# Performance work log

Hardware: AMD Instinct MI355X
Metric: run time of the kernel (lower is better)

The kernel has to match this reference:

```python
import jax, jax.numpy as jnp
import numpy as np

N_NODES = 100000
N_EDGES = 2000000


def _mlp3(h, w1, b1, w2, b2, w3, b3):
    h = jax.nn.relu(h @ w1.T + b1)
    h = jax.nn.relu(h @ w2.T + b2)
    return h @ w3.T + b3


def setup_inputs() -> dict:
    key = jax.random.key(0)
    ks = jax.random.split(key, 24)
    inp = {
        "x": jax.random.normal(ks[0], (N_NODES, 3), dtype=jnp.float32),
        "edge_index": jax.random.randint(ks[1], (2, N_EDGES), 0, N_NODES, dtype=jnp.int64),
        "edge_attr": jax.random.normal(ks[2], (N_EDGES, 4), dtype=jnp.float32),
    }
    # MLP params (PyTorch Linear: y = x @ W.T + b)
    shapes = {
        "r1_w1": (40, 10), "r1_b1": (40,), "r1_w2": (40, 40), "r1_b2": (40,), "r1_w3": (4, 40), "r1_b3": (4,),
        "o_w1": (40, 7), "o_b1": (40,), "o_w2": (40, 40), "o_b2": (40,), "o_w3": (3, 40), "o_b3": (3,),
        "r2_w1": (40, 10), "r2_b1": (40,), "r2_w2": (40, 40), "r2_b2": (40,), "r2_w3": (1, 40), "r2_b3": (1,),
    }
    for i, (name, shp) in enumerate(shapes.items()):
        inp[name] = jax.random.normal(ks[3 + i], shp, dtype=jnp.float32) * 0.1
    return inp


def reference(x, edge_index, edge_attr,
              r1_w1, r1_b1, r1_w2, r1_b2, r1_w3, r1_b3,
              o_w1, o_b1, o_w2, o_b2, o_w3, o_b3,
              r2_w1, r2_b1, r2_w2, r2_b2, r2_w3, r2_b3):
    n = x.shape[0]
    src, dst = edge_index[0], edge_index[1]  # x_j <- src, x_i <- dst
    # message: relational MLP R1 over [x_i, x_j, edge_attr]  -> [E,4]
    m1 = jnp.concatenate([x[dst], x[src], edge_attr], axis=1)
    e_msg = _mlp3(m1, r1_w1, r1_b1, r1_w2, r1_b2, r1_w3, r1_b3)
    # aggregate: scatter-add messages to destination nodes -> [N,4]
    aggr = jax.ops.segment_sum(e_msg, dst, num_segments=n)
    # update: object MLP O over [x, aggr] -> [N,3]
    x_tilde = _mlp3(jnp.concatenate([x, aggr], axis=1), o_w1, o_b1, o_w2, o_b2, o_w3, o_b3)
    # edge classifier R2 over [x_tilde_i, x_tilde_j, E] -> sigmoid [E,1]
    m2 = jnp.concatenate([x_tilde[dst], x_tilde[src], e_msg], axis=1)
    return jax.nn.sigmoid(_mlp3(m2, r2_w1, r2_b1, r2_w2, r2_b2, r2_w3, r2_b3))
```

## Files before the change

kernel.cpp:

```cpp
#include <hip/hip_runtime.h>
#include <math.h>


typedef __fp16 hf8 __attribute__((ext_vector_type(8)));
typedef _Float16 f16x2 __attribute__((ext_vector_type(2)));
typedef float f32x16 __attribute__((ext_vector_type(16)));
typedef unsigned u32x4 __attribute__((ext_vector_type(4)));

#define NEPC  64
#define BS    4096

__device__ __forceinline__ f32x16 mfma16(hf8 a, hf8 b, f32x16 c) {
    return __builtin_amdgcn_mfma_f32_32x32x16_f16(a, b, c, 0, 0, 0);
}
__device__ __forceinline__ unsigned pk2(float a, float b) {
    return __builtin_bit_cast(unsigned, __builtin_amdgcn_cvt_pkrtz(a, b));
}
__device__ __forceinline__ unsigned pk2_relu(float a, float b) {
    return __builtin_bit_cast(unsigned,
        __builtin_amdgcn_cvt_pkrtz(fmaxf(a, 0.f), fmaxf(b, 0.f)));
}
__device__ __forceinline__ unsigned pswap(unsigned v) {
    return (unsigned)__shfl_xor((int)v, 32, 64);
}
__device__ __forceinline__ hf8 frag_from(unsigned a, unsigned b, unsigned c, unsigned d) {
    u32x4 v = {a, b, c, d};
    return __builtin_bit_cast(hf8, v);
}

__device__ __forceinline__ void build_frags(const f32x16& t0, const f32x16& t1,
                                            int hi, hf8& F0, hf8& F1, hf8& F2) {
    const unsigned w0 = pk2_relu(t0[0],  t0[1]);
    const unsigned w1 = pk2_relu(t0[2],  t0[3]);
    const unsigned w2 = pk2_relu(t0[4],  t0[5]);
    const unsigned w3 = pk2_relu(t0[6],  t0[7]);
    const unsigned w4 = pk2_relu(t0[8],  t0[9]);
    const unsigned w5 = pk2_relu(t0[10], t0[11]);
    const unsigned w6 = pk2_relu(t0[12], t0[13]);
    const unsigned w7 = pk2_relu(t0[14], t0[15]);
    const unsigned w8 = pk2_relu(t1[0],  t1[1]);
    const unsigned w9 = pk2_relu(t1[2],  t1[3]);
    const unsigned p0 = pswap(w0), p1 = pswap(w1), p2 = pswap(w2), p3 = pswap(w3);
    const unsigned p4 = pswap(w4), p5 = pswap(w5), p6 = pswap(w6), p7 = pswap(w7);
    const unsigned p8 = pswap(w8), p9 = pswap(w9);
    F0 = frag_from(hi ? p2 : w0, hi ? p3 : w1, hi ? w2 : p0, hi ? w3 : p1);
    F1 = frag_from(hi ? p6 : w4, hi ? p7 : w5, hi ? w6 : p4, hi ? w7 : p5);
    F2 = frag_from(hi ? 0x00003c00u : w8, hi ? 0u : w9, hi ? 0u : p8, hi ? 0u : p9);
}

template<int IN, int OUT>
__device__ hf8 load_wfrag(const float* __restrict__ w, const float* __restrict__ b,
                          int mt, int ks, int lane) {
    const int r = mt * 32 + (lane & 31);
    const int kbase = ks * 16 + ((lane >> 5) & 1) * 8;
    hf8 f;
#pragma unroll
    for (int j = 0; j < 8; ++j) {
        const int k = kbase + j;
        float v = 0.f;
        if (r < OUT) {
            if (k < IN) v = w[r * IN + k];
            else if (k == IN) v = b[r];
        }
        f[j] = (__fp16)v;
    }
    return f;
}

template<int OUT>
__device__ hf8 load_wfrag_l1(const float* __restrict__ w, const float* __restrict__ b,
                             int mt, int lane) {
    const int r = mt * 32 + (lane & 31);
    const int kbase = ((lane >> 5) & 1) * 8;
    hf8 f;
#pragma unroll
    for (int j = 0; j < 8; ++j) {
        const int k = kbase + j;
        float v = 0.f;
        if (r < OUT) {
            int src = -1;
            if (k < 3) src = k;
            else if (k >= 4 && k < 7) src = k - 1;
            else if (k >= 8 && k < 12) src = k - 2;
            if (src >= 0) v = w[r * 10 + src];
            else if (k == 12) v = b[r];
        }
        f[j] = (__fp16)v;
    }
    return f;
}

template<bool IS_MSG>
__global__ __launch_bounds__(256, 2) void edge_kernel(
    const uint2* __restrict__ nodef,
    const int*   __restrict__ ei,
    const void*  __restrict__ eattr,
    const float* __restrict__ w1, const float* __restrict__ b1,
    const float* __restrict__ w2, const float* __restrict__ b2,
    const float* __restrict__ w3, const float* __restrict__ b3,
    uint2* __restrict__ emsg_out,
    float* __restrict__ out,
    int n_edges)
{
    const int lane = threadIdx.x & 63;
    const int ecol = lane & 31;
    const int hi = lane >> 5;

    hf8 wa1[2], wa2[2][3], wa3[3];
#pragma unroll
    for (int t = 0; t < 2; ++t) wa1[t] = load_wfrag_l1<40>(w1, b1, t, lane);
#pragma unroll
    for (int t = 0; t < 2; ++t)
#pragma unroll
        for (int s = 0; s < 3; ++s) wa2[t][s] = load_wfrag<40, 40>(w2, b2, t, s, lane);
#pragma unroll
    for (int s = 0; s < 3; ++s)
        wa3[s] = load_wfrag<40, (IS_MSG ? 4 : 1)>(w3, b3, 0, s, lane);

    const int gwave = (int)((blockIdx.x * blockDim.x + threadIdx.x) >> 6);
    const int nwave = (int)((gridDim.x * blockDim.x) >> 6);
    const int nchunk = (n_edges + NEPC - 1) / NEPC;
    const int last = n_edges - 1;

    int c = gwave;
    if (c >= nchunk) return;
    auto eclampX = [&](int cc) { int e = cc * NEPC + ecol;      return e < last ? e : last; };
    auto eclampY = [&](int cc) { int e = cc * NEPC + 32 + ecol; return e < last ? e : last; };

    uint2 fAX, fBX, fAY, fBY;
    int sNX = 0, dNX = 0, sNY = 0, dNY = 0;
    {
        const int eX = eclampX(c), eY = eclampY(c);
        if (hi == 0) {
            const int sX = ei[eX], dX = ei[n_edges + eX];
            const int sY = ei[eY], dY = ei[n_edges + eY];
            fAX = nodef[dX]; fBX = nodef[sX];
            fAY = nodef[dY]; fBY = nodef[sY];
            const int e2X = eclampX(c + nwave), e2Y = eclampY(c + nwave);
            sNX = ei[e2X]; dNX = ei[n_edges + e2X];
            sNY = ei[e2Y]; dNY = ei[n_edges + e2Y];
        } else {
            if (IS_MSG) {
                const float4 evX = ((const float4*)eattr)[eX];
                fAX = make_uint2(pk2(evX.x, evX.y), pk2(evX.z, evX.w));
                const float4 evY = ((const float4*)eattr)[eY];
                fAY = make_uint2(pk2(evY.x, evY.y), pk2(evY.z, evY.w));
            } else {
                fAX = ((const uint2*)eattr)[eX];
                fAY = ((const uint2*)eattr)[eY];
            }
            fBX = make_uint2(0x00003c00u, 0u);
            fBY = fBX;
        }
    }

    for (; c < nchunk; ) {
        const int cn = c + nwave;

        const hf8 bfX = frag_from(fAX.x, fAX.y, fBX.x, fBX.y);
        const hf8 bfY = frag_from(fAY.x, fAY.y, fBY.x, fBY.y);

        uint2 nfAX = fAX, nfBX = fBX, nfAY = fAY, nfBY = fBY;
        int sPX = sNX, dPX = dNX, sPY = sNY, dPY = dNY;
        {
            if (hi == 0) {
                nfAX = nodef[dNX]; nfBX = nodef[sNX];
                nfAY = nodef[dNY]; nfBY = nodef[sNY];
                const int e3X = eclampX(cn + nwave), e3Y = eclampY(cn + nwave);
                sPX = ei[e3X]; dPX = ei[n_edges + e3X];
                sPY = ei[e3Y]; dPY = ei[n_edges + e3Y];
            } else {
                const int e2X = eclampX(cn), e2Y = eclampY(cn);
                if (IS_MSG) {
                    const float4 evX = ((const float4*)eattr)[e2X];
                    nfAX = make_uint2(pk2(evX.x, evX.y), pk2(evX.z, evX.w));
                    const float4 evY = ((const float4*)eattr)[e2Y];
                    nfAY = make_uint2(pk2(evY.x, evY.y), pk2(evY.z, evY.w));
                } else {
                    nfAX = ((const uint2*)eattr)[e2X];
                    nfAY = ((const uint2*)eattr)[e2Y];
                }
            }
        }

        f32x16 a0X = {}, a1X = {}, a0Y = {}, a1Y = {};
        a0X = mfma16(wa1[0], bfX, a0X);
        a0Y = mfma16(wa1[0], bfY, a0Y);
        a1X = mfma16(wa1[1], bfX, a1X);
        a1Y = mfma16(wa1[1], bfY, a1Y);

        hf8 f0X, f1X, f2X, f0Y, f1Y, f2Y;
        build_frags(a0X, a1X, hi, f0X, f1X, f2X);
        build_frags(a0Y, a1Y, hi, f0Y, f1Y, f2Y);

        f32x16 c0X = {}, c1X = {}, c0Y = {}, c1Y = {};
        c0X = mfma16(wa2[0][0], f0X, c0X); c0Y = mfma16(wa2[0][0], f0Y, c0Y);
        c1X = mfma16(wa2[1][0], f0X, c1X); c1Y = mfma16(wa2[1][0], f0Y, c1Y);
        c0X = mfma16(wa2[0][1], f1X, c0X); c0Y = mfma16(wa2[0][1], f1Y, c0Y);
        c1X = mfma16(wa2[1][1], f1X, c1X); c1Y = mfma16(wa2[1][1], f1Y, c1Y);
        c0X = mfma16(wa2[0][2], f2X, c0X); c0Y = mfma16(wa2[0][2], f2Y, c0Y);
        c1X = mfma16(wa2[1][2], f2X, c1X); c1Y = mfma16(wa2[1][2], f2Y, c1Y);

        hf8 g0X, g1X, g2X, g0Y, g1Y, g2Y;
        build_frags(c0X, c1X, hi, g0X, g1X, g2X);
        build_frags(c0Y, c1Y, hi, g0Y, g1Y, g2Y);

        f32x16 z0X = {}, z0Y = {};
        z0X = mfma16(wa3[0], g0X, z0X); z0Y = mfma16(wa3[0], g0Y, z0Y);
        z0X = mfma16(wa3[1], g1X, z0X); z0Y = mfma16(wa3[1], g1Y, z0Y);
        z0X = mfma16(wa3[2], g2X, z0X); z0Y = mfma16(wa3[2], g2Y, z0Y);

        if (hi == 0) {
            const int eX = c * NEPC + ecol;
            const int eY = eX + 32;
            if (eX < n_edges) {
                if (IS_MSG)
                    emsg_out[eX] = make_uint2(pk2(z0X[0], z0X[1]), pk2(z0X[2], z0X[3]));
                else
                    out[eX] = 1.f / (1.f + expf(-z0X[0]));
            }
            if (eY < n_edges) {
                if (IS_MSG)
                    emsg_out[eY] = make_uint2(pk2(z0Y[0], z0Y[1]), pk2(z0Y[2], z0Y[3]));
                else
                    out[eY] = 1.f / (1.f + expf(-z0Y[0]));
            }
        }

        fAX = nfAX; fBX = nfBX; fAY = nfAY; fBY = nfBY;
        sNX = sPX; dNX = dPX; sNY = sPY; dNY = dPY;
        c = cn;
    }
}

__global__ __launch_bounds__(256) void nodef_kernel(
    const float* __restrict__ x, uint2* __restrict__ nodef, int n_nodes)
{
    int n = blockIdx.x * blockDim.x + threadIdx.x;
    if (n >= n_nodes) return;
    nodef[n] = make_uint2(pk2(x[n * 3 + 0], x[n * 3 + 1]), pk2(x[n * 3 + 2], 0.f));
}

__device__ __forceinline__ void bin_accum(float* __restrict__ bin, int bbase, int d,
                                          const uint2* __restrict__ emsg, long long e) {
    const unsigned nl = (unsigned)(d - bbase);
    if (nl < (unsigned)BS) {
        const uint2 mv = emsg[e];
        f16x2 lo = __builtin_bit_cast(f16x2, mv.x);
        f16x2 hi = __builtin_bit_cast(f16x2, mv.y);
        float* p = bin + nl * 4;
        atomicAdd(p + 0, (float)lo.x);
        atomicAdd(p + 1, (float)lo.y);
        atomicAdd(p + 2, (float)hi.x);
        atomicAdd(p + 3, (float)hi.y);
    }
}

__global__ __launch_bounds__(1024) void bin_kernel(
    const int* __restrict__ ei,
    const uint2* __restrict__ emsg,
    float* __restrict__ scratch,
    int n_edges, int nw)
{
    __shared__ float bin[BS * 4];
    const int B = gridDim.x / nw;
    const int wchunk = blockIdx.x / B;
    const int b = blockIdx.x % B;
    const int bbase = b * BS;
    const int tid = threadIdx.x;

#pragma unroll
    for (int i = 0; i < (BS * 4) / 1024; ++i)
        bin[tid + i * 1024] = 0.f;
    __syncthreads();

    long long e0 = ((long long)n_edges * wchunk / nw) & ~3LL;
    long long e1 = (wchunk == nw - 1) ? (long long)n_edges
                                      : (((long long)n_edges * (wchunk + 1) / nw) & ~3LL);
    const long long nfull = (e1 - e0) >> 2;
    const int* dstp = ei + n_edges;

    for (long long g = tid; g < nfull; g += 1024) {
        const long long e = e0 + g * 4;
        const int4 d4 = *(const int4*)(dstp + e);
        bin_accum(bin, bbase, d4.x, emsg, e + 0);
        bin_accum(bin, bbase, d4.y, emsg, e + 1);
        bin_accum(bin, bbase, d4.z, emsg, e + 2);
        bin_accum(bin, bbase, d4.w, emsg, e + 3);
    }
    for (long long e = e0 + nfull * 4 + tid; e < e1; e += 1024)
        bin_accum(bin, bbase, dstp[e], emsg, e);

    __syncthreads();

    float4* dst = (float4*)(scratch + ((size_t)(b * nw + wchunk)) * BS * 4);
    const float4* srcb = (const float4*)bin;
#pragma unroll
    for (int i = 0; i < (BS * 4) / 4 / 1024; ++i)
        dst[tid + i * 1024] = srcb[tid + i * 1024];
}

__global__ __launch_bounds__(256) void reduce_kernel(
    const float* __restrict__ scratch,
    float* __restrict__ aggr,
    int n_nodes, int nw)
{
    int n = blockIdx.x * blockDim.x + threadIdx.x;
    if (n >= n_nodes) return;
    const int b = n / BS, nl = n % BS;
    float4 acc = make_float4(0.f, 0.f, 0.f, 0.f);
    for (int w = 0; w < nw; ++w) {
        const float4 v = *(const float4*)(scratch + ((size_t)(b * nw + w) * BS + nl) * 4);
        acc.x += v.x; acc.y += v.y; acc.z += v.z; acc.w += v.w;
    }
    *(float4*)(aggr + (size_t)n * 4) = acc;
}

template<int IN, int OUT, bool RELU>
__device__ __forceinline__ void dense(const float* __restrict__ w,
                                      const float* __restrict__ b,
                                      const float* in, float* out) {
#pragma unroll
    for (int j = 0; j < OUT; ++j) {
        float acc = b[j];
#pragma unroll
        for (int k = 0; k < IN; ++k) acc = fmaf(w[j * IN + k], in[k], acc);
        out[j] = RELU ? fmaxf(acc, 0.f) : acc;
    }
}

__global__ __launch_bounds__(256) void node_kernel(
    const float* __restrict__ x,
    const float* __restrict__ aggr,
    const float* __restrict__ w1, const float* __restrict__ b1,
    const float* __restrict__ w2, const float* __restrict__ b2,
    const float* __restrict__ w3, const float* __restrict__ b3,
    uint2* __restrict__ xth,
    int n_nodes)
{
    int n = blockIdx.x * blockDim.x + threadIdx.x;
    if (n >= n_nodes) return;

    float in[7];
    in[0] = x[n * 3 + 0]; in[1] = x[n * 3 + 1]; in[2] = x[n * 3 + 2];
    const float4 ag = *(const float4*)(aggr + (size_t)n * 4);
    in[3] = ag.x; in[4] = ag.y; in[5] = ag.z; in[6] = ag.w;

    float h1[40], h2[40], o[3];
    dense<7, 40, true >(w1, b1, in, h1);
    dense<40, 40, true>(w2, b2, h1, h2);
    dense<40, 3, false>(w3, b3, h2, o);

    xth[n] = make_uint2(pk2(o[0], o[1]), pk2(o[2], 0.f));
}

extern "C" void kernel_launch(void* const* d_in, const int* in_sizes, int n_in,
                              void* d_out, int out_size, void* d_ws, size_t ws_size,
                              hipStream_t stream) {
    const float* x  = (const float*)d_in[0];
    const int*   ei = (const int*)d_in[1];
    const float* ea = (const float*)d_in[2];

    const float* r1_w1 = (const float*)d_in[3];
    const float* r1_b1 = (const float*)d_in[4];
    const float* r1_w2 = (const float*)d_in[5];
    const float* r1_b2 = (const float*)d_in[6];
    const float* r1_w3 = (const float*)d_in[7];
    const float* r1_b3 = (const float*)d_in[8];

    const float* o_w1 = (const float*)d_in[9];
    const float* o_b1 = (const float*)d_in[10];
    const float* o_w2 = (const float*)d_in[11];
    const float* o_b2 = (const float*)d_in[12];
    const float* o_w3 = (const float*)d_in[13];
    const float* o_b3 = (const float*)d_in[14];

    const float* r2_w1 = (const float*)d_in[15];
    const float* r2_b1 = (const float*)d_in[16];
    const float* r2_w2 = (const float*)d_in[17];
    const float* r2_b2 = (const float*)d_in[18];
    const float* r2_w3 = (const float*)d_in[19];
    const float* r2_b3 = (const float*)d_in[20];

    const int n_nodes = in_sizes[0] / 3;
    const int n_edges = in_sizes[2] / 4;
    const int B = (n_nodes + BS - 1) / BS;

    uint2* nodef   = (uint2*)d_ws;
    float* aggr    = (float*)(nodef + n_nodes);
    uint2* emsg    = (uint2*)(aggr + (size_t)n_nodes * 4);
    float* scratch = (float*)(emsg + n_edges);

    const size_t fixed_bytes = (size_t)n_nodes * 8 + (size_t)n_nodes * 16
                             + (size_t)n_edges * 8;
    int nw = 16;
    if (ws_size < fixed_bytes + (size_t)B * nw * BS * 4 * sizeof(float)) nw = 8;

    const int eb = 512;
    const int nb = (n_nodes + 255) / 256;

    nodef_kernel<<<nb, 256, 0, stream>>>(x, nodef, n_nodes);

    edge_kernel<true><<<eb, 256, 0, stream>>>(nodef, ei, (const void*)ea,
        r1_w1, r1_b1, r1_w2, r1_b2, r1_w3, r1_b3,
        emsg, nullptr, n_edges);

    bin_kernel<<<B * nw, 1024, 0, stream>>>(ei, emsg, scratch, n_edges, nw);

    reduce_kernel<<<nb, 256, 0, stream>>>(scratch, aggr, n_nodes, nw);

    node_kernel<<<nb, 256, 0, stream>>>(x, aggr,
        o_w1, o_b1, o_w2, o_b2, o_w3, o_b3, nodef, n_nodes);

    edge_kernel<false><<<eb, 256, 0, stream>>>(nodef, ei, (const void*)emsg,
        r2_w1, r2_b1, r2_w2, r2_b2, r2_w3, r2_b3,
        nullptr, (float*)d_out, n_edges);
}
```

Before: 195.3 us.

## Replace filtered scan binning with counting-sort bucketing before shared-memory scatter-add

```diff
diff --git a/kernel.cpp b/kernel.cpp
--- a/kernel.cpp
+++ b/kernel.cpp
@@ -9,6 +9,7 @@
 
 #define NEPC  64
 #define BS    4096
+#define NBMAX 32
 
 __device__ __forceinline__ f32x16 mfma16(hf8 a, hf8 b, f32x16 c) {
     return __builtin_amdgcn_mfma_f32_32x32x16_f16(a, b, c, 0, 0, 0);
@@ -233,6 +234,11 @@
     }
 }
 
+__global__ __launch_bounds__(64) void zero_small(unsigned* __restrict__ p, int n) {
+    int i = threadIdx.x;
+    if (i < n) p[i] = 0u;
+}
+
 __global__ __launch_bounds__(256) void nodef_kernel(
     const float* __restrict__ x, uint2* __restrict__ nodef, int n_nodes)
 {
@@ -241,59 +247,112 @@
     nodef[n] = make_uint2(pk2(x[n * 3 + 0], x[n * 3 + 1]), pk2(x[n * 3 + 2], 0.f));
 }
 
-__device__ __forceinline__ void bin_accum(float* __restrict__ bin, int bbase, int d,
-                                          const uint2* __restrict__ emsg, long long e) {
-    const unsigned nl = (unsigned)(d - bbase);
-    if (nl < (unsigned)BS) {
-        const uint2 mv = emsg[e];
-        f16x2 lo = __builtin_bit_cast(f16x2, mv.x);
-        f16x2 hi = __builtin_bit_cast(f16x2, mv.y);
-        float* p = bin + nl * 4;
+__global__ __launch_bounds__(1024) void count_kernel(
+    const int* __restrict__ dstp, unsigned* __restrict__ counts, int n_edges)
+{
+    __shared__ unsigned lc[NBMAX];
+    if (threadIdx.x < NBMAX) lc[threadIdx.x] = 0u;
+    __syncthreads();
+    const int stride = gridDim.x * 1024;
+    for (int e = blockIdx.x * 1024 + threadIdx.x; e < n_edges; e += stride)
+        atomicAdd(&lc[((unsigned)dstp[e]) >> 12], 1u);
+    __syncthreads();
+    if (threadIdx.x < NBMAX && lc[threadIdx.x])
+        atomicAdd(&counts[threadIdx.x], lc[threadIdx.x]);
+}
+
+__global__ __launch_bounds__(1024) void split_kernel(
+    const int* __restrict__ dstp,
+    const uint2* __restrict__ emsg,
+    const unsigned* __restrict__ counts,
+    unsigned* __restrict__ cursor,
+    unsigned* __restrict__ buckets,
+    int n_edges, int nbins)
+{
+    __shared__ unsigned lcnt[NBMAX], loff[NBMAX], gbase[NBMAX], gcnt[NBMAX];
+    __shared__ unsigned stage[1024 * 3];
+    const int tid = threadIdx.x;
+    const int e = blockIdx.x * 1024 + tid;
+    const bool valid = e < n_edges;
+
+    if (tid < NBMAX) { lcnt[tid] = 0u; gcnt[tid] = (tid < nbins) ? counts[tid] : 0u; }
+    __syncthreads();
+
+    unsigned d = 0, b = 0, slot = 0; uint2 m = make_uint2(0u, 0u);
+    if (valid) {
+        d = (unsigned)dstp[e];
+        m = emsg[e];
+        b = d >> 12;
+        slot = atomicAdd(&lcnt[b], 1u);
+    }
+    __syncthreads();
+
+    if (tid == 0) {
+        unsigned run = 0, gpre = 0;
+        for (int i = 0; i < nbins; ++i) {
+            loff[i] = run; run += lcnt[i];
+            gbase[i] = gpre + atomicAdd(&cursor[i], lcnt[i]);
+            gpre += gcnt[i];
+        }
+    }
+    __syncthreads();
+
+    if (valid) {
+        const unsigned p = (loff[b] + slot) * 3;
+        stage[p] = d; stage[p + 1] = m.x; stage[p + 2] = m.y;
+    }
+    __syncthreads();
+
+    const int total = min(1024, n_edges - blockIdx.x * 1024);
+    if (tid < total) {
+        const unsigned dd = stage[tid * 3];
+        const unsigned bb = dd >> 12;
+        const unsigned gpos = gbase[bb] + ((unsigned)tid - loff[bb]);
+        unsigned* o = buckets + (size_t)gpos * 3;
+        o[0] = dd; o[1] = stage[tid * 3 + 1]; o[2] = stage[tid * 3 + 2];
+    }
+}
+
+__global__ __launch_bounds__(1024) void accum_kernel(
+    const unsigned* __restrict__ buckets,
+    const unsigned* __restrict__ counts,
+    float* __restrict__ scratch,
+    int nbins, int S)
+{
+    __shared__ float bin[BS * 4];
+    __shared__ unsigned seg[2];
+    const int bid = blockIdx.x / S, s = blockIdx.x % S;
+    const int tid = threadIdx.x;
+
+#pragma unroll
+    for (int i = 0; i < (BS * 4) / 1024; ++i)
+        bin[tid + i * 1024] = 0.f;
+    if (tid == 0) {
+        unsigned start = 0;
+        for (int i = 0; i < bid; ++i) start += counts[i];
+        seg[0] = start; seg[1] = counts[bid];
+    }
+    __syncthreads();
+
+    const unsigned start = seg[0], len = seg[1];
+    const unsigned r0 = start + (unsigned)((unsigned long long)len * s / S);
+    const unsigned r1 = start + (unsigned)((unsigned long long)len * (s + 1) / S);
+    for (unsigned r = r0 + tid; r < r1; r += 1024) {
+        const unsigned* rec = buckets + (size_t)r * 3;
+        const unsigned d   = rec[0];
+        const unsigned m01 = rec[1];
+        const unsigned m23 = rec[2];
+        const f16x2 lo = __builtin_bit_cast(f16x2, m01);
+        const f16x2 hi = __builtin_bit_cast(f16x2, m23);
+        float* p = bin + (d & (BS - 1)) * 4;
         atomicAdd(p + 0, (float)lo.x);
         atomicAdd(p + 1, (float)lo.y);
         atomicAdd(p + 2, (float)hi.x);
         atomicAdd(p + 3, (float)hi.y);
     }
-}
-
-__global__ __launch_bounds__(1024) void bin_kernel(
-    const int* __restrict__ ei,
-    const uint2* __restrict__ emsg,
-    float* __restrict__ scratch,
-    int n_edges, int nw)
-{
-    __shared__ float bin[BS * 4];
-    const int B = gridDim.x / nw;
-    const int wchunk = blockIdx.x / B;
-    const int b = blockIdx.x % B;
-    const int bbase = b * BS;
-    const int tid = threadIdx.x;
-
-#pragma unroll
-    for (int i = 0; i < (BS * 4) / 1024; ++i)
-        bin[tid + i * 1024] = 0.f;
-    __syncthreads();
-
-    long long e0 = ((long long)n_edges * wchunk / nw) & ~3LL;
-    long long e1 = (wchunk == nw - 1) ? (long long)n_edges
-                                      : (((long long)n_edges * (wchunk + 1) / nw) & ~3LL);
-    const long long nfull = (e1 - e0) >> 2;
-    const int* dstp = ei + n_edges;
-
-    for (long long g = tid; g < nfull; g += 1024) {
-        const long long e = e0 + g * 4;
-        const int4 d4 = *(const int4*)(dstp + e);
-        bin_accum(bin, bbase, d4.x, emsg, e + 0);
-        bin_accum(bin, bbase, d4.y, emsg, e + 1);
-        bin_accum(bin, bbase, d4.z, emsg, e + 2);
-        bin_accum(bin, bbase, d4.w, emsg, e + 3);
-    }
-    for (long long e = e0 + nfull * 4 + tid; e < e1; e += 1024)
-        bin_accum(bin, bbase, dstp[e], emsg, e);
-
-    __syncthreads();
-
-    float4* dst = (float4*)(scratch + ((size_t)(b * nw + wchunk)) * BS * 4);
+    __syncthreads();
+
+    float4* dst = (float4*)(scratch + ((size_t)(bid * S + s)) * BS * 4);
     const float4* srcb = (const float4*)bin;
 #pragma unroll
     for (int i = 0; i < (BS * 4) / 4 / 1024; ++i)
@@ -386,18 +445,24 @@
     const int n_edges = in_sizes[2] / 4;
     const int B = (n_nodes + BS - 1) / BS;
 
-    uint2* nodef   = (uint2*)d_ws;
-    float* aggr    = (float*)(nodef + n_nodes);
-    uint2* emsg    = (uint2*)(aggr + (size_t)n_nodes * 4);
-    float* scratch = (float*)(emsg + n_edges);
-
-    const size_t fixed_bytes = (size_t)n_nodes * 8 + (size_t)n_nodes * 16
-                             + (size_t)n_edges * 8;
-    int nw = 16;
-    if (ws_size < fixed_bytes + (size_t)B * nw * BS * 4 * sizeof(float)) nw = 8;
+    uint2*    nodef   = (uint2*)d_ws;
+    float*    aggr    = (float*)(nodef + n_nodes);
+    uint2*    emsg    = (uint2*)(aggr + (size_t)n_nodes * 4);
+    unsigned* buckets = (unsigned*)(emsg + n_edges);
+    unsigned* counts  = buckets + (size_t)n_edges * 3;
+    unsigned* cursor  = counts + NBMAX;
+    float*    scratch = (float*)(cursor + NBMAX);
+
+    const size_t fixed_bytes = (char*)scratch - (char*)d_ws;
+    int S = 16;
+    while (S > 4 && ws_size < fixed_bytes + (size_t)B * S * BS * 4 * sizeof(float))
+        S >>= 1;
 
     const int eb = 512;
     const int nb = (n_nodes + 255) / 256;
+    const int sb = (n_edges + 1023) / 1024;
+
+    zero_small<<<1, 64, 0, stream>>>(counts, 2 * NBMAX);
 
     nodef_kernel<<<nb, 256, 0, stream>>>(x, nodef, n_nodes);
 
@@ -405,9 +470,14 @@
         r1_w1, r1_b1, r1_w2, r1_b2, r1_w3, r1_b3,
         emsg, nullptr, n_edges);
 
-    bin_kernel<<<B * nw, 1024, 0, stream>>>(ei, emsg, scratch, n_edges, nw);
-
-    reduce_kernel<<<nb, 256, 0, stream>>>(scratch, aggr, n_nodes, nw);
+    count_kernel<<<512, 1024, 0, stream>>>(ei + n_edges, counts, n_edges);
+
+    split_kernel<<<sb, 1024, 0, stream>>>(ei + n_edges, emsg, counts, cursor,
+                                          buckets, n_edges, B);
+
+    accum_kernel<<<B * S, 1024, 0, stream>>>(buckets, counts, scratch, B, S);
+
+    reduce_kernel<<<nb, 256, 0, stream>>>(scratch, aggr, n_nodes, S);
 
     node_kernel<<<nb, 256, 0, stream>>>(x, aggr,
         o_w1, o_b1, o_w2, o_b2, o_w3, o_b3, nodef, n_nodes);
```

After: 626.6 us. 3.21x slower.
